# Performance work log

Hardware: AMD Instinct MI355X
Metric: run time of the kernel (lower is better)

The kernel has to match this reference:

```python
import jax, jax.numpy as jnp
import numpy as np

B, H, L, N = 8, 128, 4096, 64
EPS = 1e-7
LOG_DT_MIN, LOG_DT_MAX = np.log(0.001), np.log(0.1)


def setup_inputs() -> dict:
    key = jax.random.key(0)
    k_u, k_lre, k_w, k_step = jax.random.split(key, 4)
    u = jax.random.normal(k_u, (B, H, L), dtype=jnp.float32)
    # HiPPO-style diagonal init: Re(Lambda) < 0 for stability, Im(Lambda) = pi*n
    Lambda_re = -0.5 * jnp.ones((H, N), jnp.float32) \
        - 0.1 * jax.random.uniform(k_lre, (H, N), dtype=jnp.float32)
    Lambda_im = jnp.broadcast_to(jnp.pi * jnp.arange(N, dtype=jnp.float32), (H, N))
    # W stored as (real, imag) pairs, stddev sqrt(0.5) per the module's initializer
    W_ri = (0.5 ** 0.5) * jax.random.normal(k_w, (H, N, 2), dtype=jnp.float32)
    D = jnp.ones((H,), jnp.float32)
    # log_step ~ U[log(1e-3), log(1e-1)] per log_step_initializer
    log_step = jax.random.uniform(k_step, (H,), dtype=jnp.float32) \
        * (LOG_DT_MAX - LOG_DT_MIN) + LOG_DT_MIN
    return {"u": u, "Lambda_re": Lambda_re, "Lambda_im": Lambda_im,
            "W_ri": W_ri, "D": D, "log_step": log_step}


def _dss_kernel(W, Lambda, step, Lseq):
    # P[h,n,l] = step_h * Lambda_hn * l
    pos = jnp.arange(Lseq, dtype=jnp.float32)
    P = (step[:, None] * Lambda)[..., None] * pos          # [H,N,L] complex64
    # complex softmax over l, stabilized by the entry with largest real part
    idx = jnp.argmax(P.real, axis=-1)[..., None]           # [H,N,1]
    e = jnp.exp(P - jnp.take_along_axis(P, idx, axis=-1))
    s = jnp.sum(e, axis=-1, keepdims=True)
    S = e * (jnp.conj(s) / (s * jnp.conj(s) + EPS))        # e / s, eps-regularized
    return jnp.einsum('hn,hnl->hl', W / Lambda, S).real    # [H,L]


def reference(u, Lambda_re, Lambda_im, W_ri, D, log_step):
    Lambda = Lambda_re + 1j * Lambda_im                    # [H,N]
    W = W_ri[..., 0] + 1j * W_ri[..., 1]                   # [H,N]
    step = jnp.exp(log_step)                               # [H]
    Lseq = u.shape[-1]
    K = _dss_kernel(W, Lambda, step, Lseq)                 # [H,L]
    # FFT-based causal convolution, zero-padded to 2L
    n = 2 * Lseq
    uf = jnp.fft.rfft(u, n=n, axis=-1)                     # [B,H,L+1]
    Kf = jnp.fft.rfft(K, n=n, axis=-1)                     # [H,L+1]
    y = jnp.fft.irfft(uf * Kf[None], n=n, axis=-1)[..., :Lseq]
    return y + D[None, :, None] * u
```

## Files before the change

kernel.cpp:

```cpp
#include <hip/hip_runtime.h>
#include <math.h>

#define H_  128
#define N_  64
#define L_  4096
#define B_  8
#define LC  128
#define NCH 32

typedef _Float16 f16;
typedef _Float16 half8 __attribute__((ext_vector_type(8)));
typedef _Float16 f16x4 __attribute__((ext_vector_type(4)));
typedef _Float16 f16x2 __attribute__((ext_vector_type(2)));
typedef float    floatx4 __attribute__((ext_vector_type(4)));

#define WS_T 0
#define WS_G ((size_t)H_*LC*LC*2)
#define WS_M ((size_t)2*H_*LC*LC*2)
#define WS_Q ((size_t)3*H_*LC*LC*2)

__device__ __forceinline__ void dss_consts(int h, int n,
    const float* __restrict__ Lre, const float* __restrict__ Lim,
    const float* __restrict__ Wri, const float* __restrict__ lstep,
    float& af, float& bf, float& crf, float& cif, float& qrf, float& qif)
{
    const float stepf = expf(lstep[h]);
    const float a  = stepf * Lre[h*N_ + n];
    const float bp = stepf * Lim[h*N_ + n];
    const double ad = (double)a, bd = (double)bp;
    const double em = exp(ad);
    const double rre = em * cos(bd), rim = em * sin(bd);
    const double eL = exp(ad * (double)L_);
    const double rLre = eL * cos(bd * (double)L_), rLim = eL * sin(bd * (double)L_);
    const double nre = 1.0 - rLre, nim = -rLim;
    const double dre = 1.0 - rre,  dim = -rim;
    const double dm  = dre*dre + dim*dim;
    const double sre = (nre*dre + nim*dim) / dm;
    const double sim = (nim*dre - nre*dim) / dm;
    const double wre = (double)Wri[(h*N_ + n)*2 + 0];
    const double wim = (double)Wri[(h*N_ + n)*2 + 1];
    const double lre = (double)Lre[h*N_ + n], lim = (double)Lim[h*N_ + n];
    const double lm  = lre*lre + lim*lim;
    const double wor = (wre*lre + wim*lim) / lm;
    const double woi = (wim*lre - wre*lim) / lm;
    const double sm  = sre*sre + sim*sim + 1e-7;
    const double eC  = exp(ad * (double)LC);
    af = a; bf = bp;
    crf = (float)((wor*sre + woi*sim) / sm);
    cif = (float)((woi*sre - wor*sim) / sm);
    qrf = (float)(eC * cos(bd * (double)LC));
    qif = (float)(eC * sin(bd * (double)LC));
}

__global__ __launch_bounds__(256)
void dss_prep(const float* __restrict__ Lre, const float* __restrict__ Lim,
              const float* __restrict__ Wri, const float* __restrict__ Dv,
              const float* __restrict__ lstep, char* __restrict__ ws)
{
    __shared__ float s_a[N_], s_b[N_], s_cr[N_], s_ci[N_];
    __shared__ float sKp[2][128];
    __shared__ float sK[128];
    const int h = blockIdx.x;
    const int which = blockIdx.y;
    const int t = threadIdx.x;

    if (t < N_) {
        float a, b, cr, ci, qr, qi;
        dss_consts(h, t, Lre, Lim, Wri, lstep, a, b, cr, ci, qr, qi);
        s_a[t] = a; s_b[t] = b; s_cr[t] = cr; s_ci[t] = ci;
        if (which == 0) {
            float* qg = (float*)(ws + WS_Q) + (size_t)h*N_*2;
            qg[2*t] = qr; qg[2*t+1] = qi;
        }
    }
    __syncthreads();

    if (which == 0) {
        const int tt = t & 127, hf = t >> 7;
        float acc = 0.f;
        #pragma unroll
        for (int m = 0; m < 32; ++m) {
            const int n = hf*32 + m;
            const float ex = expf(s_a[n] * (float)tt);
            float sn, cs; sincosf(s_b[n] * (float)tt, &sn, &cs);
            acc = fmaf(ex, s_cr[n]*cs - s_ci[n]*sn, acc);
        }
        sKp[hf][tt] = acc;
        __syncthreads();
        if (t < 128) {
            float kv = sKp[0][t] + sKp[1][t];
            if (t == 0) kv += Dv[h];
            sK[t] = kv;
        }
        __syncthreads();
        f16* Tg = (f16*)(ws + WS_T) + (size_t)h*LC*LC;
        #pragma unroll
        for (int i = 0; i < 8; ++i) {
            const int e8 = t + i*256;
            const int row = e8 >> 4, c0 = (e8 & 15) * 8;
            half8 pv;
            #pragma unroll
            for (int j = 0; j < 8; ++j) {
                const int col = c0 + j;
                pv[j] = (f16)((row >= col) ? sK[row - col] : 0.f);
            }
            *reinterpret_cast<half8*>(&Tg[row*LC + c0]) = pv;
        }
    } else if (which == 1) {
        f16* Gg = (f16*)(ws + WS_G) + (size_t)h*LC*LC;
        #pragma unroll
        for (int i = 0; i < 8; ++i) {
            const int e8 = t + i*256;
            const int row = e8 >> 4, c0 = (e8 & 15) * 8;
            const int m = row >> 1, im = row & 1;
            const float a = s_a[m], b = s_b[m];
            half8 pv;
            #pragma unroll
            for (int j = 0; j < 8; ++j) {
                const float p = (float)(127 - (c0 + j));
                const float ex = expf(a * p);
                float sn, cs; sincosf(b * p, &sn, &cs);
                pv[j] = (f16)(im ? ex*sn : ex*cs);
            }
            *reinterpret_cast<half8*>(&Gg[row*LC + c0]) = pv;
        }
    } else {
        f16* Mg = (f16*)(ws + WS_M) + (size_t)h*LC*LC;
        #pragma unroll
        for (int i = 0; i < 8; ++i) {
            const int e8 = t + i*256;
            const int row = e8 >> 4, c0 = (e8 & 15) * 8;
            const float p = (float)(row + 1);
            half8 pv;
            #pragma unroll
            for (int mm = 0; mm < 4; ++mm) {
                const int m = (c0 >> 1) + mm;
                const float ex = expf(s_a[m] * p);
                float sn, cs; sincosf(s_b[m] * p, &sn, &cs);
                const float pr = ex*cs, pi = ex*sn;
                pv[2*mm]   = (f16)( 16.f * (s_cr[m]*pr - s_ci[m]*pi));
                pv[2*mm+1] = (f16)(-16.f * (s_cr[m]*pi + s_ci[m]*pr));
            }
            *reinterpret_cast<half8*>(&Mg[row*LC + c0]) = pv;
        }
    }
}

__global__ __launch_bounds__(256, 4)
void dss_main(const float* __restrict__ u, const char* __restrict__ ws,
              float* __restrict__ out)
{
    __shared__ f16   sU[NCH][132];
    __shared__ float sE[NCH][132];
    __shared__ f16   sC[NCH][132];

    const int t  = threadIdx.x;
    const int bh = blockIdx.x;
    const int h  = bh & (H_-1);
    const f16* Tg = (const f16*)(ws + WS_T) + (size_t)h*LC*LC;
    const f16* Gg = (const f16*)(ws + WS_G) + (size_t)h*LC*LC;
    const f16* Mg = (const f16*)(ws + WS_M) + (size_t)h*LC*LC;
    const float* qg = (const float*)(ws + WS_Q) + (size_t)h*N_*2;

    {
        const float4* up = reinterpret_cast<const float4*>(u + (size_t)bh * L_);
        #pragma unroll
        for (int i = 0; i < L_/4/256; ++i) {
            const int e4 = t + i*256;
            const float4 v = up[e4];
            const int row = e4 >> 5, c4 = (e4 & 31) * 4;
            f16x4 pv = { (f16)v.x, (f16)v.y, (f16)v.z, (f16)v.w };
            *reinterpret_cast<f16x4*>(&sU[row][c4]) = pv;
        }
    }
    __syncthreads();

    const int w  = t >> 6;
    const int l  = t & 63;
    const int lr = l & 15;
    const int lg = l >> 4;

    floatx4 accA[2][2] = {};
    floatx4 accB[2][2] = {};

    #pragma unroll
    for (int ks = 0; ks < 4; ++ks) {
        const int ko = ks*32 + lg*8;
        const half8 a0 = *reinterpret_cast<const half8*>(&sU[lr     ][ko]);
        const half8 a1 = *reinterpret_cast<const half8*>(&sU[16 + lr][ko]);
        #pragma unroll
        for (int nt = 0; nt < 2; ++nt) {
            const int ncol = (2*w + nt)*16 + lr;
            const half8 bT = *reinterpret_cast<const half8*>(&Tg[ncol*LC + ko]);
            const half8 bG = *reinterpret_cast<const half8*>(&Gg[ncol*LC + ko]);
            accA[0][nt] = __builtin_amdgcn_mfma_f32_16x16x32_f16(a0, bT, accA[0][nt], 0, 0, 0);
            accA[1][nt] = __builtin_amdgcn_mfma_f32_16x16x32_f16(a1, bT, accA[1][nt], 0, 0, 0);
            accB[0][nt] = __builtin_amdgcn_mfma_f32_16x16x32_f16(a0, bG, accB[0][nt], 0, 0, 0);
            accB[1][nt] = __builtin_amdgcn_mfma_f32_16x16x32_f16(a1, bG, accB[1][nt], 0, 0, 0);
        }
    }
    #pragma unroll
    for (int mt = 0; mt < 2; ++mt)
        #pragma unroll
        for (int nt = 0; nt < 2; ++nt)
            #pragma unroll
            for (int j = 0; j < 4; ++j)
                sE[mt*16 + lg*4 + j][(2*w + nt)*16 + lr] = accB[mt][nt][j];
    __syncthreads();

    if (w == 0) {
        const float qre = qg[2*l], qim = qg[2*l+1];
        float cr = 0.f, ci = 0.f;
        #pragma unroll
        for (int k = 0; k < NCH; ++k) {
            const float er = sE[k][2*l], ei = sE[k][2*l+1];
            *reinterpret_cast<f16x2*>(&sC[k][2*l]) =
                (f16x2){ (f16)(cr * 0.0625f), (f16)(ci * 0.0625f) };
            const float ncr = fmaf(qre, cr, fmaf(-qim, ci, er));
            const float nci = fmaf(qre, ci, fmaf( qim, cr, ei));
            cr = ncr; ci = nci;
        }
    }
    __syncthreads();

    #pragma unroll
    for (int ks = 0; ks < 4; ++ks) {
        const int ko = ks*32 + lg*8;
        const half8 a0 = *reinterpret_cast<const half8*>(&sC[lr     ][ko]);
        const half8 a1 = *reinterpret_cast<const half8*>(&sC[16 + lr][ko]);
        #pragma unroll
        for (int nt = 0; nt < 2; ++nt) {
            const int ncol = (2*w + nt)*16 + lr;
            const half8 bM = *reinterpret_cast<const half8*>(&Mg[ncol*LC + ko]);
            accA[0][nt] = __builtin_amdgcn_mfma_f32_16x16x32_f16(a0, bM, accA[0][nt], 0, 0, 0);
            accA[1][nt] = __builtin_amdgcn_mfma_f32_16x16x32_f16(a1, bM, accA[1][nt], 0, 0, 0);
        }
    }

    #pragma unroll
    for (int mt = 0; mt < 2; ++mt)
        #pragma unroll
        for (int nt = 0; nt < 2; ++nt)
            #pragma unroll
            for (int j = 0; j < 4; ++j)
                sE[mt*16 + lg*4 + j][(2*w + nt)*16 + lr] = accA[mt][nt][j];
    __syncthreads();
    {
        float4* op = reinterpret_cast<float4*>(out + (size_t)bh * L_);
        #pragma unroll
        for (int i = 0; i < L_/4/256; ++i) {
            const int e4 = t + i*256;
            const int row = e4 >> 5, c4 = (e4 & 31) * 4;
            op[e4] = *reinterpret_cast<const float4*>(&sE[row][c4]);
        }
    }
}

extern "C" void kernel_launch(void* const* d_in, const int* in_sizes, int n_in,
                              void* d_out, int out_size, void* d_ws, size_t ws_size,
                              hipStream_t stream) {
    const float* u  = (const float*)d_in[0];
    const float* lr = (const float*)d_in[1];
    const float* li = (const float*)d_in[2];
    const float* w  = (const float*)d_in[3];
    const float* dv = (const float*)d_in[4];
    const float* ls = (const float*)d_in[5];
    float* out = (float*)d_out;
    char* ws = (char*)d_ws;
    dss_prep<<<dim3(H_, 3), dim3(256), 0, stream>>>(lr, li, w, dv, ls, ws);
    dss_main<<<dim3(B_*H_), dim3(256), 0, stream>>>(u, ws, out);
}
```

Before: 105.6 us.

## Fuse prep and main kernels, build matrices in LDS, loop over batch per block

Merges the prep and main kernels into a single kernel. Each block builds the Toeplitz, G and M matrices for one head directly in shared memory and then processes four batch slices, prefetching the next slice of u into registers while computing the current one. This removes the workspace round trip, one kernel launch, and the global loads of the matrices in the main phase. In exchange, only 256 blocks run at one block per CU with large LDS use, and each block repeats the matrix construction for its head, which costs parallelism and duplicated transcendental work.

```diff
diff --git a/kernel.cpp b/kernel.cpp
--- a/kernel.cpp
+++ b/kernel.cpp
@@ -7,17 +7,15 @@
 #define B_  8
 #define LC  128
 #define NCH 32
+#define SPB 4
+#define RS  136
+#define RSE 132
 
 typedef _Float16 f16;
 typedef _Float16 half8 __attribute__((ext_vector_type(8)));
 typedef _Float16 f16x4 __attribute__((ext_vector_type(4)));
 typedef _Float16 f16x2 __attribute__((ext_vector_type(2)));
 typedef float    floatx4 __attribute__((ext_vector_type(4)));
-
-#define WS_T 0
-#define WS_G ((size_t)H_*LC*LC*2)
-#define WS_M ((size_t)2*H_*LC*LC*2)
-#define WS_Q ((size_t)3*H_*LC*LC*2)
 
 __device__ __forceinline__ void dss_consts(int h, int n,
     const float* __restrict__ Lre, const float* __restrict__ Lim,
@@ -52,66 +50,75 @@
     qif = (float)(eC * sin(bd * (double)LC));
 }
 
-__global__ __launch_bounds__(256)
-void dss_prep(const float* __restrict__ Lre, const float* __restrict__ Lim,
-              const float* __restrict__ Wri, const float* __restrict__ Dv,
-              const float* __restrict__ lstep, char* __restrict__ ws)
+__global__ __launch_bounds__(256, 1)
+void dss_fused(const float* __restrict__ u,
+               const float* __restrict__ Lre, const float* __restrict__ Lim,
+               const float* __restrict__ Wri, const float* __restrict__ Dv,
+               const float* __restrict__ lstep, float* __restrict__ out)
 {
+    __shared__ f16   sT[LC][RS];
+    __shared__ f16   sG[LC][RS];
+    __shared__ f16   sM[LC][RS];
+    __shared__ f16   sU[2][NCH][RS];
+    __shared__ float sE[NCH][RSE];
+    __shared__ f16   sC[NCH][RS];
+    __shared__ float sKp[2][LC];
+    __shared__ float sK[LC];
+    __shared__ float sQ[2*N_];
     __shared__ float s_a[N_], s_b[N_], s_cr[N_], s_ci[N_];
-    __shared__ float sKp[2][128];
-    __shared__ float sK[128];
-    const int h = blockIdx.x;
-    const int which = blockIdx.y;
+
     const int t = threadIdx.x;
+    const int h = blockIdx.x >> 1;
+    const int s = blockIdx.x & 1;
+
+    float4 fr0, fr1, fr2, fr3;
+    {
+        const float4* up = reinterpret_cast<const float4*>(u + ((size_t)(s*SPB)*H_ + h) * L_);
+        fr0 = up[t]; fr1 = up[t+256]; fr2 = up[t+512]; fr3 = up[t+768];
+    }
 
     if (t < N_) {
         float a, b, cr, ci, qr, qi;
         dss_consts(h, t, Lre, Lim, Wri, lstep, a, b, cr, ci, qr, qi);
-        s_a[t] = a; s_b[t] = b; s_cr[t] = cr; s_ci[t] = ci;
-        if (which == 0) {
-            float* qg = (float*)(ws + WS_Q) + (size_t)h*N_*2;
-            qg[2*t] = qr; qg[2*t+1] = qi;
-        }
+        s_a[t]=a; s_b[t]=b; s_cr[t]=cr; s_ci[t]=ci;
+        sQ[2*t]=qr; sQ[2*t+1]=qi;
     }
     __syncthreads();
 
-    if (which == 0) {
-        const int tt = t & 127, hf = t >> 7;
+    {
+        const int lag = t & 127, hf = t >> 7;
         float acc = 0.f;
         #pragma unroll
         for (int m = 0; m < 32; ++m) {
             const int n = hf*32 + m;
-            const float ex = expf(s_a[n] * (float)tt);
-            float sn, cs; sincosf(s_b[n] * (float)tt, &sn, &cs);
+            const float ex = expf(s_a[n] * (float)lag);
+            float sn, cs; sincosf(s_b[n] * (float)lag, &sn, &cs);
             acc = fmaf(ex, s_cr[n]*cs - s_ci[n]*sn, acc);
         }
-        sKp[hf][tt] = acc;
-        __syncthreads();
-        if (t < 128) {
-            float kv = sKp[0][t] + sKp[1][t];
-            if (t == 0) kv += Dv[h];
-            sK[t] = kv;
-        }
-        __syncthreads();
-        f16* Tg = (f16*)(ws + WS_T) + (size_t)h*LC*LC;
-        #pragma unroll
-        for (int i = 0; i < 8; ++i) {
-            const int e8 = t + i*256;
-            const int row = e8 >> 4, c0 = (e8 & 15) * 8;
+        sKp[hf][lag] = acc;
+    }
+    __syncthreads();
+    if (t < LC) {
+        float kv = sKp[0][t] + sKp[1][t];
+        if (t == 0) kv += Dv[h];
+        sK[t] = kv;
+    }
+    __syncthreads();
+
+    #pragma unroll
+    for (int i = 0; i < 8; ++i) {
+        const int e8 = t + i*256;
+        const int row = e8 >> 4, c0 = (e8 & 15) * 8;
+        {
             half8 pv;
             #pragma unroll
             for (int j = 0; j < 8; ++j) {
                 const int col = c0 + j;
                 pv[j] = (f16)((row >= col) ? sK[row - col] : 0.f);
             }
-            *reinterpret_cast<half8*>(&Tg[row*LC + c0]) = pv;
-        }
-    } else if (which == 1) {
-        f16* Gg = (f16*)(ws + WS_G) + (size_t)h*LC*LC;
-        #pragma unroll
-        for (int i = 0; i < 8; ++i) {
-            const int e8 = t + i*256;
-            const int row = e8 >> 4, c0 = (e8 & 15) * 8;
+            *reinterpret_cast<half8*>(&sT[row][c0]) = pv;
+        }
+        {
             const int m = row >> 1, im = row & 1;
             const float a = s_a[m], b = s_b[m];
             half8 pv;
@@ -122,14 +129,9 @@
                 float sn, cs; sincosf(b * p, &sn, &cs);
                 pv[j] = (f16)(im ? ex*sn : ex*cs);
             }
-            *reinterpret_cast<half8*>(&Gg[row*LC + c0]) = pv;
-        }
-    } else {
-        f16* Mg = (f16*)(ws + WS_M) + (size_t)h*LC*LC;
-        #pragma unroll
-        for (int i = 0; i < 8; ++i) {
-            const int e8 = t + i*256;
-            const int row = e8 >> 4, c0 = (e8 & 15) * 8;
+            *reinterpret_cast<half8*>(&sG[row][c0]) = pv;
+        }
+        {
             const float p = (float)(row + 1);
             half8 pv;
             #pragma unroll
@@ -141,117 +143,107 @@
                 pv[2*mm]   = (f16)( 16.f * (s_cr[m]*pr - s_ci[m]*pi));
                 pv[2*mm+1] = (f16)(-16.f * (s_cr[m]*pi + s_ci[m]*pr));
             }
-            *reinterpret_cast<half8*>(&Mg[row*LC + c0]) = pv;
-        }
-    }
-}
-
-__global__ __launch_bounds__(256, 4)
-void dss_main(const float* __restrict__ u, const char* __restrict__ ws,
-              float* __restrict__ out)
-{
-    __shared__ f16   sU[NCH][132];
-    __shared__ float sE[NCH][132];
-    __shared__ f16   sC[NCH][132];
-
-    const int t  = threadIdx.x;
-    const int bh = blockIdx.x;
-    const int h  = bh & (H_-1);
-    const f16* Tg = (const f16*)(ws + WS_T) + (size_t)h*LC*LC;
-    const f16* Gg = (const f16*)(ws + WS_G) + (size_t)h*LC*LC;
-    const f16* Mg = (const f16*)(ws + WS_M) + (size_t)h*LC*LC;
-    const float* qg = (const float*)(ws + WS_Q) + (size_t)h*N_*2;
-
-    {
-        const float4* up = reinterpret_cast<const float4*>(u + (size_t)bh * L_);
-        #pragma unroll
-        for (int i = 0; i < L_/4/256; ++i) {
-            const int e4 = t + i*256;
-            const float4 v = up[e4];
-            const int row = e4 >> 5, c4 = (e4 & 31) * 4;
-            f16x4 pv = { (f16)v.x, (f16)v.y, (f16)v.z, (f16)v.w };
-            *reinterpret_cast<f16x4*>(&sU[row][c4]) = pv;
-        }
-    }
-    __syncthreads();
+            *reinterpret_cast<half8*>(&sM[row][c0]) = pv;
+        }
+    }
 
     const int w  = t >> 6;
     const int l  = t & 63;
     const int lr = l & 15;
     const int lg = l >> 4;
 
-    floatx4 accA[2][2] = {};
-    floatx4 accB[2][2] = {};
-
     #pragma unroll
-    for (int ks = 0; ks < 4; ++ks) {
-        const int ko = ks*32 + lg*8;
-        const half8 a0 = *reinterpret_cast<const half8*>(&sU[lr     ][ko]);
-        const half8 a1 = *reinterpret_cast<const half8*>(&sU[16 + lr][ko]);
-        #pragma unroll
-        for (int nt = 0; nt < 2; ++nt) {
-            const int ncol = (2*w + nt)*16 + lr;
-            const half8 bT = *reinterpret_cast<const half8*>(&Tg[ncol*LC + ko]);
-            const half8 bG = *reinterpret_cast<const half8*>(&Gg[ncol*LC + ko]);
-            accA[0][nt] = __builtin_amdgcn_mfma_f32_16x16x32_f16(a0, bT, accA[0][nt], 0, 0, 0);
-            accA[1][nt] = __builtin_amdgcn_mfma_f32_16x16x32_f16(a1, bT, accA[1][nt], 0, 0, 0);
-            accB[0][nt] = __builtin_amdgcn_mfma_f32_16x16x32_f16(a0, bG, accB[0][nt], 0, 0, 0);
-            accB[1][nt] = __builtin_amdgcn_mfma_f32_16x16x32_f16(a1, bG, accB[1][nt], 0, 0, 0);
-        }
-    }
-    #pragma unroll
-    for (int mt = 0; mt < 2; ++mt)
-        #pragma unroll
-        for (int nt = 0; nt < 2; ++nt)
-            #pragma unroll
-            for (int j = 0; j < 4; ++j)
-                sE[mt*16 + lg*4 + j][(2*w + nt)*16 + lr] = accB[mt][nt][j];
-    __syncthreads();
-
-    if (w == 0) {
-        const float qre = qg[2*l], qim = qg[2*l+1];
-        float cr = 0.f, ci = 0.f;
-        #pragma unroll
-        for (int k = 0; k < NCH; ++k) {
-            const float er = sE[k][2*l], ei = sE[k][2*l+1];
-            *reinterpret_cast<f16x2*>(&sC[k][2*l]) =
-                (f16x2){ (f16)(cr * 0.0625f), (f16)(ci * 0.0625f) };
-            const float ncr = fmaf(qre, cr, fmaf(-qim, ci, er));
-            const float nci = fmaf(qre, ci, fmaf( qim, cr, ei));
-            cr = ncr; ci = nci;
-        }
-    }
-    __syncthreads();
-
-    #pragma unroll
-    for (int ks = 0; ks < 4; ++ks) {
-        const int ko = ks*32 + lg*8;
-        const half8 a0 = *reinterpret_cast<const half8*>(&sC[lr     ][ko]);
-        const half8 a1 = *reinterpret_cast<const half8*>(&sC[16 + lr][ko]);
-        #pragma unroll
-        for (int nt = 0; nt < 2; ++nt) {
-            const int ncol = (2*w + nt)*16 + lr;
-            const half8 bM = *reinterpret_cast<const half8*>(&Mg[ncol*LC + ko]);
-            accA[0][nt] = __builtin_amdgcn_mfma_f32_16x16x32_f16(a0, bM, accA[0][nt], 0, 0, 0);
-            accA[1][nt] = __builtin_amdgcn_mfma_f32_16x16x32_f16(a1, bM, accA[1][nt], 0, 0, 0);
-        }
-    }
-
-    #pragma unroll
-    for (int mt = 0; mt < 2; ++mt)
-        #pragma unroll
-        for (int nt = 0; nt < 2; ++nt)
-            #pragma unroll
-            for (int j = 0; j < 4; ++j)
-                sE[mt*16 + lg*4 + j][(2*w + nt)*16 + lr] = accA[mt][nt][j];
-    __syncthreads();
-    {
-        float4* op = reinterpret_cast<float4*>(out + (size_t)bh * L_);
-        #pragma unroll
-        for (int i = 0; i < L_/4/256; ++i) {
-            const int e4 = t + i*256;
+    for (int i = 0; i < SPB; ++i) {
+        const int cur = i & 1;
+
+        #pragma unroll
+        for (int j = 0; j < 4; ++j) {
+            const float4 v = (j==0)?fr0:(j==1)?fr1:(j==2)?fr2:fr3;
+            const int e4 = t + j*256;
             const int row = e4 >> 5, c4 = (e4 & 31) * 4;
-            op[e4] = *reinterpret_cast<const float4*>(&sE[row][c4]);
+            f16x4 pv = { (f16)v.x, (f16)v.y, (f16)v.z, (f16)v.w };
+            *reinterpret_cast<f16x4*>(&sU[cur][row][c4]) = pv;
+        }
+        if (i < SPB-1) {
+            const float4* up = reinterpret_cast<const float4*>(
+                u + ((size_t)(s*SPB + i + 1)*H_ + h) * L_);
+            fr0 = up[t]; fr1 = up[t+256]; fr2 = up[t+512]; fr3 = up[t+768];
+        }
+        __syncthreads();
+
+        floatx4 accA[2][2] = {};
+        floatx4 accB[2][2] = {};
+
+        #pragma unroll
+        for (int ks = 0; ks < 4; ++ks) {
+            const int ko = ks*32 + lg*8;
+            const half8 a0 = *reinterpret_cast<const half8*>(&sU[cur][lr     ][ko]);
+            const half8 a1 = *reinterpret_cast<const half8*>(&sU[cur][16 + lr][ko]);
+            #pragma unroll
+            for (int nt = 0; nt < 2; ++nt) {
+                const int ncol = (2*w + nt)*16 + lr;
+                const half8 bT = *reinterpret_cast<const half8*>(&sT[ncol][ko]);
+                const half8 bG = *reinterpret_cast<const half8*>(&sG[ncol][ko]);
+                accA[0][nt] = __builtin_amdgcn_mfma_f32_16x16x32_f16(a0, bT, accA[0][nt], 0, 0, 0);
+                accA[1][nt] = __builtin_amdgcn_mfma_f32_16x16x32_f16(a1, bT, accA[1][nt], 0, 0, 0);
+                accB[0][nt] = __builtin_amdgcn_mfma_f32_16x16x32_f16(a0, bG, accB[0][nt], 0, 0, 0);
+                accB[1][nt] = __builtin_amdgcn_mfma_f32_16x16x32_f16(a1, bG, accB[1][nt], 0, 0, 0);
+            }
+        }
+        #pragma unroll
+        for (int mt = 0; mt < 2; ++mt)
+            #pragma unroll
+            for (int nt = 0; nt < 2; ++nt)
+                #pragma unroll
+                for (int j = 0; j < 4; ++j)
+                    sE[mt*16 + lg*4 + j][(2*w + nt)*16 + lr] = accB[mt][nt][j];
+        __syncthreads();
+
+        if (w == 0) {
+            const float qre = sQ[2*l], qim = sQ[2*l+1];
+            float cr = 0.f, ci = 0.f;
+            #pragma unroll
+            for (int k = 0; k < NCH; ++k) {
+                const float er = sE[k][2*l], ei = sE[k][2*l+1];
+                *reinterpret_cast<f16x2*>(&sC[k][2*l]) =
+                    (f16x2){ (f16)(cr * 0.0625f), (f16)(ci * 0.0625f) };
+                const float ncr = fmaf(qre, cr, fmaf(-qim, ci, er));
+                const float nci = fmaf(qre, ci, fmaf( qim, cr, ei));
+                cr = ncr; ci = nci;
+            }
+        }
+        __syncthreads();
+
+        #pragma unroll
+        for (int ks = 0; ks < 4; ++ks) {
+            const int ko = ks*32 + lg*8;
+            const half8 a0 = *reinterpret_cast<const half8*>(&sC[lr     ][ko]);
+            const half8 a1 = *reinterpret_cast<const half8*>(&sC[16 + lr][ko]);
+            #pragma unroll
+            for (int nt = 0; nt < 2; ++nt) {
+                const int ncol = (2*w + nt)*16 + lr;
+                const half8 bM = *reinterpret_cast<const half8*>(&sM[ncol][ko]);
+                accA[0][nt] = __builtin_amdgcn_mfma_f32_16x16x32_f16(a0, bM, accA[0][nt], 0, 0, 0);
+                accA[1][nt] = __builtin_amdgcn_mfma_f32_16x16x32_f16(a1, bM, accA[1][nt], 0, 0, 0);
+            }
+        }
+
+        #pragma unroll
+        for (int mt = 0; mt < 2; ++mt)
+            #pragma unroll
+            for (int nt = 0; nt < 2; ++nt)
+                #pragma unroll
+                for (int j = 0; j < 4; ++j)
+                    sE[mt*16 + lg*4 + j][(2*w + nt)*16 + lr] = accA[mt][nt][j];
+        __syncthreads();
+        {
+            float4* op = reinterpret_cast<float4*>(out + ((size_t)(s*SPB + i)*H_ + h) * L_);
+            #pragma unroll
+            for (int j = 0; j < 4; ++j) {
+                const int e4 = t + j*256;
+                const int row = e4 >> 5, c4 = (e4 & 31) * 4;
+                op[e4] = *reinterpret_cast<const float4*>(&sE[row][c4]);
+            }
         }
     }
 }
@@ -266,7 +258,5 @@
     const float* dv = (const float*)d_in[4];
     const float* ls = (const float*)d_in[5];
     float* out = (float*)d_out;
-    char* ws = (char*)d_ws;
-    dss_prep<<<dim3(H_, 3), dim3(256), 0, stream>>>(lr, li, w, dv, ls, ws);
-    dss_main<<<dim3(B_*H_), dim3(256), 0, stream>>>(u, ws, out);
+    dss_fused<<<dim3(H_*2), dim3(256), 0, stream>>>(u, lr, li, w, dv, ls, out);
 }
```

After: 136.3 us. 1.29x slower.
